# Performance work log

Measured on AMD Instinct MI355X. Metric: run time of the kernel, lower is better.

Reference implementation:

```python
import jax, jax.numpy as jnp
import numpy as np

N = 50000        # nodes
E = 800000       # edges (before self-loops)
F_IN = 256       # input feature dim
HID = 64         # hidden per head (concat=False -> head mean)
NCLS = 40        # classes
HEADS = 8
NEG_SLOPE = 0.2  # PyG GATConv default leaky_relu slope


def setup_inputs() -> dict:
    key = jax.random.key(0)
    ks = jax.random.split(key, 11)
    s = 0.1
    return {
        "x": jax.random.normal(ks[0], (N, F_IN), jnp.float32),
        "edge_index": jax.random.randint(ks[1], (2, E), 0, N, dtype=jnp.int64),
        "edge_attr": jax.random.uniform(ks[2], (E, 1), jnp.float32),
        "W0": jax.random.normal(ks[3], (HEADS * HID, F_IN), jnp.float32) * s,
        "a0s": jax.random.normal(ks[4], (HEADS, HID), jnp.float32) * s,
        "a0d": jax.random.normal(ks[5], (HEADS, HID), jnp.float32) * s,
        "b0": jnp.zeros((HID,), jnp.float32),
        "W2": jax.random.normal(ks[6], (HEADS * NCLS, HID), jnp.float32) * s,
        "a2s": jax.random.normal(ks[7], (HEADS, NCLS), jnp.float32) * s,
        "a2d": jax.random.normal(ks[8], (HEADS, NCLS), jnp.float32) * s,
        "b2": jnp.zeros((NCLS,), jnp.float32),
    }


def _gat_conv(x, src, dst, W, att_src, att_dst, bias, heads, out_c):
    # Linear: [N, in] @ [heads*out, in]^T -> [N, heads, out]
    h = (x @ W.T).reshape(N, heads, out_c)
    # Per-node attention logits, gathered per edge.
    a_s = jnp.einsum('nhc,hc->nh', h, att_src)
    a_d = jnp.einsum('nhc,hc->nh', h, att_dst)
    e = jax.nn.leaky_relu(a_s[src] + a_d[dst], NEG_SLOPE)  # [E, H]
    # Segment softmax over incoming edges of each destination node.
    m = jax.ops.segment_max(e, dst, num_segments=N)
    p = jnp.exp(e - m[dst])
    denom = jax.ops.segment_sum(p, dst, num_segments=N)
    alpha = p / (denom[dst] + 1e-16)
    # Weighted message scatter-sum: [E,H,C] -> [N,H,C]
    out = jax.ops.segment_sum(alpha[:, :, None] * h[src], dst, num_segments=N)
    # concat=False -> mean over heads, then bias.
    return out.mean(axis=1) + bias


def reference(x, edge_index, edge_attr, W0, a0s, a0d, b0, W2, a2s, a2d, b2):
    # edge_attr is unpacked by the torch forward but never used by GATConv.
    # PyG GATConv adds self-loops by default.
    loops = jnp.arange(N, dtype=edge_index.dtype)
    src = jnp.concatenate([edge_index[0], loops])
    dst = jnp.concatenate([edge_index[1], loops])
    h = jax.nn.relu(_gat_conv(x, src, dst, W0, a0s, a0d, b0, HEADS, HID))
    # dropout is identity in eval mode
    out = _gat_conv(h, src, dst, W2, a2s, a2d, b2, HEADS, NCLS)
    return jax.nn.log_softmax(out, axis=1)
```

## Files before the change

kernel.cpp:

```cpp
#include <hip/hip_runtime.h>
#include <hip/hip_bf16.h>
#include <math.h>


#define NEG_SLOPE 0.2f

typedef short v8s __attribute__((ext_vector_type(8)));
typedef float v4f __attribute__((ext_vector_type(4)));
typedef float v2f __attribute__((ext_vector_type(2)));
typedef unsigned short u16;
typedef unsigned int u32;
typedef unsigned char u8;

__device__ __forceinline__ u16 f2bf(float f) {
    union { float f; u32 u; } v; v.f = f;
    u32 r = v.u + 0x7fffu + ((v.u >> 16) & 1u);
    return (u16)(r >> 16);
}
__device__ __forceinline__ float lrelu_exp(float e) {
    e = (e > 0.f) ? e : NEG_SLOPE * e;
    return __expf(e);
}
__device__ __forceinline__ void dec8(uint2 r, float* h) {
    v2f a = __builtin_amdgcn_cvt_pk_f32_fp8(r.x, false);
    v2f b = __builtin_amdgcn_cvt_pk_f32_fp8(r.x, true);
    v2f c = __builtin_amdgcn_cvt_pk_f32_fp8(r.y, false);
    v2f d = __builtin_amdgcn_cvt_pk_f32_fp8(r.y, true);
    h[0] = a.x; h[1] = a.y; h[2] = b.x; h[3] = b.y;
    h[4] = c.x; h[5] = c.y; h[6] = d.x; h[7] = d.y;
}
__device__ __forceinline__ u8 enc8(float v) {
    u32 p = __builtin_amdgcn_cvt_pk_fp8_f32(v, v, 0u, false);
    return (u8)(p & 0xffu);
}


__global__ __launch_bounds__(256) void histcast_k(const int* __restrict__ ei, int* __restrict__ deg,
                                                  int E, int Nn, int NBh,
                                                  const float* __restrict__ x, u16* __restrict__ xb,
                                                  const float* __restrict__ W0, u16* __restrict__ W0b,
                                                  const float* __restrict__ W2, u16* __restrict__ W2b,
                                                  int nx, int n0c, int n2c) {
    int b = blockIdx.x;
    if (b < NBh) {
        int e = b * 256 + threadIdx.x;
        int ET = E + Nn;
        if (e >= ET) return;
        int d = (e < E) ? ei[E + e] : (e - E);
        atomicAdd(&deg[d], 1);
    } else {
        int i = ((b - NBh) * 256 + threadIdx.x) * 4;
        const float* in; u16* out;
        if (i < nx)            { in = x;  out = xb; }
        else if (i < nx + n0c) { in = W0; out = W0b; i -= nx; }
        else if (i < nx + n0c + n2c) { in = W2; out = W2b; i -= nx + n0c; }
        else return;
        float4 v = *reinterpret_cast<const float4*>(in + i);
        ushort4 o;
        o.x = f2bf(v.x); o.y = f2bf(v.y); o.z = f2bf(v.z); o.w = f2bf(v.w);
        *reinterpret_cast<ushort4*>(out + i) = o;
    }
}


__global__ __launch_bounds__(1024) void scanA_k(const int* __restrict__ deg, int* __restrict__ incl,
                                                int* __restrict__ bsum, int* __restrict__ dbin, int n) {
    __shared__ int wsum[16];
    __shared__ int dh[256];
    int t = threadIdx.x;
    if (t < 256) dh[t] = 0;
    int i = blockIdx.x * 1024 + t;
    int v = (i < n) ? deg[i] : 0;
    __syncthreads();
    if (i < n) atomicAdd(&dh[v < 255 ? v : 255], 1);
    int lane = t & 63, wid = t >> 6;
    int sv = v;
    for (int off = 1; off < 64; off <<= 1) {
        int u = __shfl_up(sv, off, 64);
        if (lane >= off) sv += u;
    }
    if (lane == 63) wsum[wid] = sv;
    __syncthreads();
    if (t < 16) {
        int w = wsum[t];
        for (int off = 1; off < 16; off <<= 1) {
            int u = __shfl_up(w, off, 64);
            if (t >= off) w += u;
        }
        wsum[t] = w;
    }
    if (t < 256 && dh[t] > 0) atomicAdd(&dbin[t], dh[t]);
    __syncthreads();
    int pre = (wid > 0) ? wsum[wid - 1] : 0;
    int inc = pre + sv;
    if (i < n) incl[i] = inc;
    if (t == 1023) bsum[blockIdx.x] = inc;
}


__global__ __launch_bounds__(256) void scanBC_k(const int* __restrict__ incl, const int* __restrict__ deg,
                                                const int* __restrict__ bsum, int* __restrict__ rowstart,
                                                int n, int B) {
    __shared__ int sb[65];
    int t = threadIdx.x;
    if (t < 64) {
        int v = (t < B) ? bsum[t] : 0;
        int sv = v;
        for (int off = 1; off < 64; off <<= 1) {
            int u = __shfl_up(sv, off, 64);
            if (t >= off) sv += u;
        }
        sb[t] = sv - v;
        if (t == 63) sb[64] = sv;
    }
    __syncthreads();
    int i = blockIdx.x * 256 + t;
    if (i < n) rowstart[i] = sb[i >> 10] + incl[i] - deg[i];
    if (i == 0) rowstart[n] = sb[64];
}


__global__ __launch_bounds__(256) void scatter_k(const int* __restrict__ ei,
                                                 const int* __restrict__ rowstart,
                                                 int* __restrict__ cursor,
                                                 int* __restrict__ srcs, int E, int Nn,
                                                 const int* __restrict__ deg,
                                                 const int* __restrict__ dbin,
                                                 int* __restrict__ dcur,
                                                 int* __restrict__ order) {
    int b = blockIdx.x, t = threadIdx.x;
    int e = b * 256 + t;
    int ET = E + Nn;
    if (e < ET) {
        int s, d;
        if (e < E) { s = ei[e]; d = ei[E + e]; }
        else       { s = e - E; d = e - E; }
        int pos = atomicAdd(&cursor[d], 1);
        srcs[rowstart[d] + pos] = s;
    }
    if (b * 256 < Nn) {
        __shared__ int ws4[4];
        __shared__ int sbase[256];
        __shared__ int lhist[256];
        __shared__ int lbase[256];
        lhist[t] = 0;
        int v = dbin[t];
        int lane = t & 63, wid = t >> 6;
        int sv = v;
        for (int off = 1; off < 64; off <<= 1) {
            int u = __shfl_up(sv, off, 64);
            if (lane >= off) sv += u;
        }
        if (lane == 63) ws4[wid] = sv;
        __syncthreads();
        int add = 0;
        for (int k = 0; k < wid; k++) add += ws4[k];
        sbase[t] = add + sv - v;
        __syncthreads();
        int i = b * 256 + t;
        int d = 0, rank = -1;
        if (i < Nn) {
            d = deg[i]; d = (d < 255) ? d : 255;
            rank = atomicAdd(&lhist[d], 1);
        }
        __syncthreads();
        int cnt = lhist[t];
        if (cnt > 0) lbase[t] = atomicAdd(&dcur[t], cnt);
        __syncthreads();
        if (i < Nn) order[sbase[d] + lbase[d] + rank] = i;
    }
}


__global__ __launch_bounds__(256, 4) void gemm_mfma(const u16* __restrict__ Ab,
                                                    const u16* __restrict__ Bb,
                                                    u8* __restrict__ Cf, int M, int Nc, int K,
                                                    const float* __restrict__ avs_vec,
                                                    const float* __restrict__ avd_vec,
                                                    float* as_out, float* ad_out) {
    __shared__ __align__(16) u8 lds[27648];
    u16 (*As)[72] = reinterpret_cast<u16(*)[72]>(lds);
    u16 (*Bs)[72] = reinterpret_cast<u16(*)[72]>(lds + 18432);
    const int t = threadIdx.x;
    const int m0 = blockIdx.x * 128;
    const int n0 = blockIdx.y * 64;
    const int w = t >> 6, lane = t & 63;
    const int wr = w * 32;
    const int q = lane >> 4, l16 = lane & 15;

    v4f acc[2][4];
#pragma unroll
    for (int i = 0; i < 2; i++)
#pragma unroll
        for (int j = 0; j < 4; j++) acc[i][j] = (v4f){0.f, 0.f, 0.f, 0.f};

    for (int kt = 0; kt < K; kt += 64) {
#pragma unroll
        for (int it = 0; it < 4; it++) {
            int c = it * 256 + t;
            int row = c >> 3, col8 = (c & 7) * 8;
            int gm = m0 + row;
            uint4 va = make_uint4(0u, 0u, 0u, 0u);
            if (gm < M) va = *reinterpret_cast<const uint4*>(Ab + (size_t)gm * K + kt + col8);
            *reinterpret_cast<uint4*>(&As[row][col8]) = va;
        }
#pragma unroll
        for (int it = 0; it < 2; it++) {
            int c = it * 256 + t;
            int row = c >> 3, col8 = (c & 7) * 8;
            uint4 vb = *reinterpret_cast<const uint4*>(Bb + (size_t)(n0 + row) * K + kt + col8);
            *reinterpret_cast<uint4*>(&Bs[row][col8]) = vb;
        }
        __syncthreads();
#pragma unroll
        for (int ks = 0; ks < 2; ks++) {
            v8s af[2], bf[4];
#pragma unroll
            for (int i = 0; i < 2; i++)
                af[i] = *reinterpret_cast<const v8s*>(&As[wr + i * 16 + l16][ks * 32 + q * 8]);
#pragma unroll
            for (int j = 0; j < 4; j++)
                bf[j] = *reinterpret_cast<const v8s*>(&Bs[j * 16 + l16][ks * 32 + q * 8]);
#pragma unroll
            for (int i = 0; i < 2; i++)
#pragma unroll
                for (int j = 0; j < 4; j++)
                    acc[i][j] = __builtin_amdgcn_mfma_f32_16x16x32_bf16(af[i], bf[j], acc[i][j], 0, 0, 0);
        }
        __syncthreads();
    }

    const bool do_att = (as_out != nullptr);
    float avs[4], avd[4];
    if (do_att) {
#pragma unroll
        for (int j = 0; j < 4; j++) {
            avs[j] = avs_vec[n0 + j * 16 + l16];
            avd[j] = avd_vec[n0 + j * 16 + l16];
        }
    }
    const int head = n0 >> 6;

    u8* Cs = lds;
#pragma unroll
    for (int i = 0; i < 2; i++) {
#pragma unroll
        for (int r = 0; r < 4; r++) {
            int row = wr + i * 16 + q * 4 + r;
#pragma unroll
            for (int j = 0; j < 4; j++)
                Cs[row * 80 + j * 16 + l16] = enc8(acc[i][j][r]);
            if (do_att) {
                int gm = m0 + row;
                float ps = 0.f, pd = 0.f;
#pragma unroll
                for (int j = 0; j < 4; j++) {
                    float v = acc[i][j][r];
                    ps = fmaf(v, avs[j], ps);
                    pd = fmaf(v, avd[j], pd);
                }
#pragma unroll
                for (int m = 1; m < 16; m <<= 1) {
                    ps += __shfl_xor(ps, m, 64);
                    pd += __shfl_xor(pd, m, 64);
                }
                if (l16 == 0 && gm < M) {
                    as_out[gm * 8 + head] = ps;
                    ad_out[gm * 8 + head] = pd;
                }
            }
        }
    }
    __syncthreads();
#pragma unroll
    for (int it = 0; it < 2; it++) {
        int idx = it * 256 + t;
        int row = idx >> 2, ch = idx & 3;
        int gm = m0 + row;
        if (gm < M)
            *reinterpret_cast<uint4*>(Cf + (size_t)gm * Nc + n0 + ch * 16) =
                *reinterpret_cast<const uint4*>(&Cs[row * 80 + ch * 16]);
    }
}


__global__ __launch_bounds__(256) void agg1_k(const u8* __restrict__ h1f,
                                              const float* __restrict__ as1, const float* __restrict__ ad1,
                                              const int* __restrict__ srcs, const int* __restrict__ rowstart,
                                              const int* __restrict__ order,
                                              const float* __restrict__ b0, u16* __restrict__ x1b, int Nn) {
    int wave = threadIdx.x >> 6, lane = threadIdx.x & 63;
    int gid = blockIdx.x * 4 + wave;
    if (gid >= Nn) return;
    int n = __builtin_amdgcn_readfirstlane(order[gid]);
    const int hl = lane >> 3;
    const float adl = ad1[n * 8 + hl];
    const u32 loff = (u32)lane * 8u;
    float acc[8] = {0, 0, 0, 0, 0, 0, 0, 0};
    float dsum = 0.f;
    int beg = rowstart[n], end = rowstart[n + 1];
    int i = beg;
    for (; i + 8 <= end; i += 8) {
        int s[8];
#pragma unroll
        for (int u = 0; u < 8; u++) s[u] = __builtin_amdgcn_readfirstlane(srcs[i + u]);
        uint2 rw[8];
#pragma unroll
        for (int u = 0; u < 8; u++) rw[u] = *reinterpret_cast<const uint2*>(h1f + ((u32)s[u] * 512u + loff));
        float eg[8];
#pragma unroll
        for (int u = 0; u < 8; u++) eg[u] = as1[(u32)s[u] * 8u + hl];
        float p[8];
#pragma unroll
        for (int u = 0; u < 8; u++) { p[u] = lrelu_exp(eg[u] + adl); dsum += p[u]; }
#pragma unroll
        for (int u = 0; u < 8; u++) {
            float hv[8];
            dec8(rw[u], hv);
#pragma unroll
            for (int j = 0; j < 8; j++) acc[j] = fmaf(p[u], hv[j], acc[j]);
        }
    }
    for (; i + 4 <= end; i += 4) {
        int s[4];
#pragma unroll
        for (int u = 0; u < 4; u++) s[u] = __builtin_amdgcn_readfirstlane(srcs[i + u]);
        uint2 rw[4];
#pragma unroll
        for (int u = 0; u < 4; u++) rw[u] = *reinterpret_cast<const uint2*>(h1f + ((u32)s[u] * 512u + loff));
        float eg[4];
#pragma unroll
        for (int u = 0; u < 4; u++) eg[u] = as1[(u32)s[u] * 8u + hl];
#pragma unroll
        for (int u = 0; u < 4; u++) {
            float p = lrelu_exp(eg[u] + adl);
            dsum += p;
            float hv[8];
            dec8(rw[u], hv);
#pragma unroll
            for (int j = 0; j < 8; j++) acc[j] = fmaf(p, hv[j], acc[j]);
        }
    }
    for (; i < end; i++) {
        int s = __builtin_amdgcn_readfirstlane(srcs[i]);
        uint2 raw = *reinterpret_cast<const uint2*>(h1f + ((u32)s * 512u + loff));
        float p = lrelu_exp(as1[(u32)s * 8u + hl] + adl);
        dsum += p;
        float hv[8];
        dec8(raw, hv);
#pragma unroll
        for (int j = 0; j < 8; j++) acc[j] = fmaf(p, hv[j], acc[j]);
    }
    float inv = 1.f / (dsum + 1e-16f);
    float r[8];
#pragma unroll
    for (int j = 0; j < 8; j++) r[j] = acc[j] * inv;
#pragma unroll
    for (int j = 0; j < 8; j++) {
        r[j] += __shfl_xor(r[j], 8, 64);
        r[j] += __shfl_xor(r[j], 16, 64);
        r[j] += __shfl_xor(r[j], 32, 64);
    }
    if (lane < 8) {
        u16 o[8];
#pragma unroll
        for (int j = 0; j < 8; j++) {
            float v = r[j] * 0.125f + b0[lane * 8 + j];
            o[j] = f2bf((v > 0.f) ? v : 0.f);
        }
        *reinterpret_cast<uint4*>(x1b + (size_t)n * 64 + lane * 8) =
            *reinterpret_cast<const uint4*>(o);
    }
}


__global__ __launch_bounds__(256) void att2_k(const u8* __restrict__ h2f,
                                              const float* __restrict__ a2s, const float* __restrict__ a2d,
                                              float* __restrict__ as2, float* __restrict__ ad2, int Nn) {
    int t = blockIdx.x * 256 + threadIdx.x;
    if (t >= Nn * 8) return;
    int n = t >> 3, h = t & 7;
    const u8* hr = h2f + (size_t)n * 320 + h * 40;
    float s1 = 0.f, s2 = 0.f;
#pragma unroll
    for (int b = 0; b < 5; b++) {
        uint2 raw = *reinterpret_cast<const uint2*>(hr + b * 8);
        float h8[8];
        dec8(raw, h8);
#pragma unroll
        for (int j = 0; j < 8; j++) {
            int c = h * 40 + b * 8 + j;
            s1 = fmaf(h8[j], a2s[c], s1);
            s2 = fmaf(h8[j], a2d[c], s2);
        }
    }
    as2[t] = s1;
    ad2[t] = s2;
}


__global__ __launch_bounds__(256) void agg2_k(const u8* __restrict__ h2f,
                                              const float* __restrict__ as2, const float* __restrict__ ad2,
                                              const int* __restrict__ srcs, const int* __restrict__ rowstart,
                                              const int* __restrict__ order,
                                              const float* __restrict__ b2, float* __restrict__ out, int Nn) {
    __shared__ float smem[4][320];
    int wave = threadIdx.x >> 6, lane = threadIdx.x & 63;
    int gid = blockIdx.x * 4 + wave;
    bool active = (gid < Nn);
    int n = 0;
    if (active) n = __builtin_amdgcn_readfirstlane(order[gid]);
    bool ld = active && (lane < 40);
    const int hl = lane / 5;
    float adl = ld ? ad2[n * 8 + hl] : 0.f;
    float acc[8] = {0, 0, 0, 0, 0, 0, 0, 0};
    float dsum = 0.f;
    if (ld) {
        const u32 loff = (u32)lane * 8u;
        int beg = rowstart[n], end = rowstart[n + 1];
        int i = beg;
        for (; i + 8 <= end; i += 8) {
            int s[8];
#pragma unroll
            for (int u = 0; u < 8; u++) s[u] = __builtin_amdgcn_readfirstlane(srcs[i + u]);
            uint2 rw[8];
#pragma unroll
            for (int u = 0; u < 8; u++) rw[u] = *reinterpret_cast<const uint2*>(h2f + ((u32)s[u] * 320u + loff));
            float eg[8];
#pragma unroll
            for (int u = 0; u < 8; u++) eg[u] = as2[(u32)s[u] * 8u + hl];
            float p[8];
#pragma unroll
            for (int u = 0; u < 8; u++) { p[u] = lrelu_exp(eg[u] + adl); dsum += p[u]; }
#pragma unroll
            for (int u = 0; u < 8; u++) {
                float hv[8];
                dec8(rw[u], hv);
#pragma unroll
                for (int j = 0; j < 8; j++) acc[j] = fmaf(p[u], hv[j], acc[j]);
            }
        }
        for (; i + 4 <= end; i += 4) {
            int s[4];
#pragma unroll
            for (int u = 0; u < 4; u++) s[u] = __builtin_amdgcn_readfirstlane(srcs[i + u]);
            uint2 rw[4];
#pragma unroll
            for (int u = 0; u < 4; u++) rw[u] = *reinterpret_cast<const uint2*>(h2f + ((u32)s[u] * 320u + loff));
            float eg[4];
#pragma unroll
            for (int u = 0; u < 4; u++) eg[u] = as2[(u32)s[u] * 8u + hl];
#pragma unroll
            for (int u = 0; u < 4; u++) {
                float p = lrelu_exp(eg[u] + adl);
                dsum += p;
                float hv[8];
                dec8(rw[u], hv);
#pragma unroll
                for (int j = 0; j < 8; j++) acc[j] = fmaf(p, hv[j], acc[j]);
            }
        }
        for (; i < end; i++) {
            int s = __builtin_amdgcn_readfirstlane(srcs[i]);
            uint2 raw = *reinterpret_cast<const uint2*>(h2f + ((u32)s * 320u + loff));
            float p = lrelu_exp(as2[(u32)s * 8u + hl] + adl);
            dsum += p;
            float hv[8];
            dec8(raw, hv);
#pragma unroll
            for (int j = 0; j < 8; j++) acc[j] = fmaf(p, hv[j], acc[j]);
        }
        float inv = 1.f / (dsum + 1e-16f);
#pragma unroll
        for (int j = 0; j < 8; j++) smem[wave][lane * 8 + j] = acc[j] * inv;
    }
    __syncthreads();
    if (active) {
        float v;
        if (lane < 40) {
            float ssum = 0.f;
#pragma unroll
            for (int h = 0; h < 8; h++) ssum += smem[wave][h * 40 + lane];
            v = ssum * 0.125f + b2[lane];
        } else {
            v = -INFINITY;
        }
        float m = v;
        for (int off = 32; off > 0; off >>= 1) m = fmaxf(m, __shfl_xor(m, off, 64));
        float ex = (lane < 40) ? __expf(v - m) : 0.f;
        float se = ex;
        for (int off = 32; off > 0; off >>= 1) se += __shfl_xor(se, off, 64);
        if (lane < 40) out[(size_t)n * 40 + lane] = v - m - __logf(se);
    }
}


extern "C" void kernel_launch(void* const* d_in, const int* in_sizes, int n_in,
                              void* d_out, int out_size, void* d_ws, size_t ws_size,
                              hipStream_t stream) {
    const float* x   = (const float*)d_in[0];
    const int*   ei  = (const int*)d_in[1];
    const float* W0  = (const float*)d_in[3];
    const float* a0s = (const float*)d_in[4];
    const float* a0d = (const float*)d_in[5];
    const float* b0  = (const float*)d_in[6];
    const float* W2  = (const float*)d_in[7];
    const float* a2s = (const float*)d_in[8];
    const float* a2d = (const float*)d_in[9];
    const float* b2  = (const float*)d_in[10];
    float* out = (float*)d_out;

    const int Nn = in_sizes[0] / 256;
    const int E  = in_sizes[1] / 2;
    const int ET = E + Nn;
    const int NB = (Nn + 1023) / 1024;

    size_t off = 0;
    auto carve = [&](size_t bytes) -> void* {
        void* p = (char*)d_ws + off;
        off += (bytes + 255) & ~(size_t)255;
        return p;
    };
    u16*   xb       = (u16*)carve((size_t)Nn * 256 * 2);
    u16*   W0b      = (u16*)carve((size_t)512 * 256 * 2);
    u16*   W2b      = (u16*)carve((size_t)320 * 64 * 2);
    u8*    h1f      = (u8*)carve((size_t)Nn * 512);
    u16*   x1b      = (u16*)carve((size_t)Nn * 64 * 2);
    u8*    h2f      = (u8*)carve((size_t)Nn * 320);
    float* as1      = (float*)carve((size_t)Nn * 8 * 4);
    float* ad1      = (float*)carve((size_t)Nn * 8 * 4);
    float* as2      = (float*)carve((size_t)Nn * 8 * 4);
    float* ad2      = (float*)carve((size_t)Nn * 8 * 4);
    int*   deg      = (int*)carve((size_t)Nn * 4);
    int*   cursor   = (int*)carve((size_t)Nn * 4);
    int*   dbin     = (int*)carve(256 * 4);
    int*   dcur     = (int*)carve(256 * 4);
    int*   rowstart = (int*)carve((size_t)(Nn + 1) * 4);
    int*   srcs     = (int*)carve((size_t)ET * 4);
    int*   incl     = (int*)carve((size_t)Nn * 4);
    int*   bsum     = (int*)carve(64 * 4);
    int*   order    = (int*)carve((size_t)Nn * 4);

    const size_t zlen = (size_t)((char*)rowstart - (char*)deg);
    hipMemsetAsync(deg, 0, zlen, stream);

    const int nx = Nn * 256, n0c = 512 * 256, n2c = 320 * 64;
    const int NBh = (ET + 255) / 256;
    const int NBc = ((nx + n0c + n2c) / 4 + 255) / 256;
    histcast_k<<<NBh + NBc, 256, 0, stream>>>(ei, deg, E, Nn, NBh,
                                              x, xb, W0, W0b, W2, W2b, nx, n0c, n2c);
    scanA_k<<<NB, 1024, 0, stream>>>(deg, incl, bsum, dbin, Nn);
    scanBC_k<<<(Nn + 255) / 256, 256, 0, stream>>>(incl, deg, bsum, rowstart, Nn, NB);
    scatter_k<<<(ET + 255) / 256, 256, 0, stream>>>(ei, rowstart, cursor, srcs, E, Nn,
                                                    deg, dbin, dcur, order);

    gemm_mfma<<<dim3((Nn + 127) / 128, 8), 256, 0, stream>>>(
        xb, W0b, h1f, Nn, 512, 256, a0s, a0d, as1, ad1);
    agg1_k<<<(Nn + 3) / 4, 256, 0, stream>>>(h1f, as1, ad1, srcs, rowstart, order, b0, x1b, Nn);

    gemm_mfma<<<dim3((Nn + 127) / 128, 5), 256, 0, stream>>>(
        x1b, W2b, h2f, Nn, 320, 64, nullptr, nullptr, nullptr, nullptr);
    att2_k<<<(Nn * 8 + 255) / 256, 256, 0, stream>>>(h2f, a2s, a2d, as2, ad2, Nn);
    agg2_k<<<(Nn + 3) / 4, 256, 0, stream>>>(h2f, as2, ad2, srcs, rowstart, order, b2, out, Nn);
}
```

Baseline: 392.4 us.

## Stage full weight tile in LDS once, stream A from global, reverse degree order

The GEMM is templated on K. The whole 64-row weight slice is loaded into LDS once, and the A fragments are read straight from global memory into registers, so the per-K-tile LDS staging and its barriers go away. The node processing order is also reversed, so aggregation blocks handle high-degree nodes first for better load balance. A rows past M are no longer bounds-checked, so the last block can read beyond the input buffer. The larger LDS footprint for K=256 may reduce occupancy.

```diff
diff --git a/kernel.cpp b/kernel.cpp
--- a/kernel.cpp
+++ b/kernel.cpp
@@ -167,20 +167,23 @@
         int cnt = lhist[t];
         if (cnt > 0) lbase[t] = atomicAdd(&dcur[t], cnt);
         __syncthreads();
-        if (i < Nn) order[sbase[d] + lbase[d] + rank] = i;
-    }
-}
-
-
+        if (i < Nn) order[Nn - 1 - (sbase[d] + lbase[d] + rank)] = i;
+    }
+}
+
+
+template<int KK>
 __global__ __launch_bounds__(256, 4) void gemm_mfma(const u16* __restrict__ Ab,
                                                     const u16* __restrict__ Bb,
-                                                    u8* __restrict__ Cf, int M, int Nc, int K,
+                                                    u8* __restrict__ Cf, int M, int Nc,
                                                     const float* __restrict__ avs_vec,
                                                     const float* __restrict__ avd_vec,
                                                     float* as_out, float* ad_out) {
-    __shared__ __align__(16) u8 lds[27648];
-    u16 (*As)[72] = reinterpret_cast<u16(*)[72]>(lds);
-    u16 (*Bs)[72] = reinterpret_cast<u16(*)[72]>(lds + 18432);
+    constexpr int SB = KK + 8;
+    constexpr int BBY = 64 * SB * 2;
+    constexpr int LBY = (BBY > 10240) ? BBY : 10240;
+    __shared__ __align__(16) u8 lds[LBY];
+    u16* Bs = reinterpret_cast<u16*>(lds);
     const int t = threadIdx.x;
     const int m0 = blockIdx.x * 128;
     const int n0 = blockIdx.y * 64;
@@ -188,46 +191,38 @@
     const int wr = w * 32;
     const int q = lane >> 4, l16 = lane & 15;
 
+    constexpr int CH = KK / 8;
+#pragma unroll
+    for (int c = t; c < 64 * CH; c += 256) {
+        int row = c / CH, ch = c % CH;
+        int gn = n0 + row;
+        uint4 vb = make_uint4(0u, 0u, 0u, 0u);
+        if (gn < Nc) vb = *reinterpret_cast<const uint4*>(Bb + (size_t)gn * KK + ch * 8);
+        *reinterpret_cast<uint4*>(&Bs[row * SB + ch * 8]) = vb;
+    }
+    __syncthreads();
+
     v4f acc[2][4];
 #pragma unroll
     for (int i = 0; i < 2; i++)
 #pragma unroll
         for (int j = 0; j < 4; j++) acc[i][j] = (v4f){0.f, 0.f, 0.f, 0.f};
 
-    for (int kt = 0; kt < K; kt += 64) {
-#pragma unroll
-        for (int it = 0; it < 4; it++) {
-            int c = it * 256 + t;
-            int row = c >> 3, col8 = (c & 7) * 8;
-            int gm = m0 + row;
-            uint4 va = make_uint4(0u, 0u, 0u, 0u);
-            if (gm < M) va = *reinterpret_cast<const uint4*>(Ab + (size_t)gm * K + kt + col8);
-            *reinterpret_cast<uint4*>(&As[row][col8]) = va;
-        }
-#pragma unroll
-        for (int it = 0; it < 2; it++) {
-            int c = it * 256 + t;
-            int row = c >> 3, col8 = (c & 7) * 8;
-            uint4 vb = *reinterpret_cast<const uint4*>(Bb + (size_t)(n0 + row) * K + kt + col8);
-            *reinterpret_cast<uint4*>(&Bs[row][col8]) = vb;
-        }
-        __syncthreads();
-#pragma unroll
-        for (int ks = 0; ks < 2; ks++) {
-            v8s af[2], bf[4];
-#pragma unroll
-            for (int i = 0; i < 2; i++)
-                af[i] = *reinterpret_cast<const v8s*>(&As[wr + i * 16 + l16][ks * 32 + q * 8]);
-#pragma unroll
-            for (int j = 0; j < 4; j++)
-                bf[j] = *reinterpret_cast<const v8s*>(&Bs[j * 16 + l16][ks * 32 + q * 8]);
-#pragma unroll
-            for (int i = 0; i < 2; i++)
-#pragma unroll
-                for (int j = 0; j < 4; j++)
-                    acc[i][j] = __builtin_amdgcn_mfma_f32_16x16x32_bf16(af[i], bf[j], acc[i][j], 0, 0, 0);
-        }
-        __syncthreads();
+    const u16* A0 = Ab + (size_t)(m0 + wr + l16) * KK + q * 8;
+    const u16* A1 = A0 + (size_t)16 * KK;
+#pragma unroll
+    for (int kc = 0; kc < KK / 32; kc++) {
+        v8s a0 = *reinterpret_cast<const v8s*>(A0 + kc * 32);
+        v8s a1 = *reinterpret_cast<const v8s*>(A1 + kc * 32);
+        v8s bf[4];
+#pragma unroll
+        for (int j = 0; j < 4; j++)
+            bf[j] = *reinterpret_cast<const v8s*>(&Bs[(j * 16 + l16) * SB + kc * 32 + q * 8]);
+#pragma unroll
+        for (int j = 0; j < 4; j++) {
+            acc[0][j] = __builtin_amdgcn_mfma_f32_16x16x32_bf16(a0, bf[j], acc[0][j], 0, 0, 0);
+            acc[1][j] = __builtin_amdgcn_mfma_f32_16x16x32_bf16(a1, bf[j], acc[1][j], 0, 0, 0);
+        }
     }
 
     const bool do_att = (as_out != nullptr);
@@ -241,6 +236,7 @@
     }
     const int head = n0 >> 6;
 
+    __syncthreads();
     u8* Cs = lds;
 #pragma unroll
     for (int i = 0; i < 2; i++) {
@@ -554,12 +550,12 @@
     scatter_k<<<(ET + 255) / 256, 256, 0, stream>>>(ei, rowstart, cursor, srcs, E, Nn,
                                                     deg, dbin, dcur, order);
 
-    gemm_mfma<<<dim3((Nn + 127) / 128, 8), 256, 0, stream>>>(
-        xb, W0b, h1f, Nn, 512, 256, a0s, a0d, as1, ad1);
+    gemm_mfma<256><<<dim3((Nn + 127) / 128, 8), 256, 0, stream>>>(
+        xb, W0b, h1f, Nn, 512, a0s, a0d, as1, ad1);
     agg1_k<<<(Nn + 3) / 4, 256, 0, stream>>>(h1f, as1, ad1, srcs, rowstart, order, b0, x1b, Nn);
 
-    gemm_mfma<<<dim3((Nn + 127) / 128, 5), 256, 0, stream>>>(
-        x1b, W2b, h2f, Nn, 320, 64, nullptr, nullptr, nullptr, nullptr);
+    gemm_mfma<64><<<dim3((Nn + 127) / 128, 5), 256, 0, stream>>>(
+        x1b, W2b, h2f, Nn, 320, nullptr, nullptr, nullptr, nullptr);
     att2_k<<<(Nn * 8 + 255) / 256, 256, 0, stream>>>(h2f, a2s, a2d, as2, ad2, Nn);
     agg2_k<<<(Nn + 3) / 4, 256, 0, stream>>>(h2f, as2, ad2, srcs, rowstart, order, b2, out, Nn);
 }
```

Result: no change. 389.8 us (-0.7%).
